# Kernel tuning notes

Measured on AMD Instinct MI355X. Metric: run time of the kernel, lower is better.

The kernel has to match this reference:

```python
import jax, jax.numpy as jnp
import numpy as np
import math

NUM_HEADS = 8
DIM = 512
HEAD_DIM = DIM // NUM_HEADS
SCALE = HEAD_DIM ** -0.5
RP = 2            # remove_pad = kernel_size//2 * 2 for kernel_size=3
EPS_GN = 1e-5     # GroupNorm eps
EPS_L1 = 1e-12    # F.normalize eps


def _conv(x, w, b):
    # x: [B, Cin, H, W], w: [Cout, Cin, 3, 3] (OIHW), VALID padding, stride 1
    y = jax.lax.conv_general_dilated(x, w, (1, 1), 'VALID',
                                     dimension_numbers=('NCHW', 'OIHW', 'NCHW'))
    return y + b[None, :, None, None]


def _gn_per_channel(x, g, b):
    # GroupNorm with num_groups == num_channels: per-channel norm over (H, W)
    mu = x.mean(axis=(-2, -1), keepdims=True)
    var = x.var(axis=(-2, -1), keepdims=True)
    xn = (x - mu) * jax.lax.rsqrt(var + EPS_GN)
    return xn * g[None, :, None, None] + b[None, :, None, None]


def _ppe(rpe, c1w, c1b, g1w, g1b, c2w, c2b, g2w, g2b):
    # PeripheralPositionEncoding: rpe [side^2, side^2, 4*H] -> [1, H, N, N], N=(side-2*RP)^2
    nr, _, d = rpe.shape
    side = int(round(math.sqrt(nr)))
    s2 = side - 2 * RP
    x = rpe.reshape(side, side, side, side, d)          # i j k l d
    x = x[RP:side - RP, RP:side - RP]                   # trim i, j borders
    x = x.transpose(0, 1, 4, 2, 3).reshape(s2 * s2, d, side, side)  # (ij) d k l
    x = jax.nn.relu(_gn_per_channel(_conv(x, c1w, c1b), g1w, g1b))
    x = _gn_per_channel(_conv(x, c2w, c2b), g2w, g2b)   # [(ij), H, s2, s2]
    y = x.reshape(s2 * s2, NUM_HEADS, s2 * s2).transpose(1, 0, 2)[None]  # [1,H,N,N]
    return jax.nn.sigmoid(y)


def setup_inputs() -> dict:
    key = jax.random.key(0)
    ks = jax.random.split(key, 12)
    B, N = 8, 1024            # N = (36 - 4)^2
    side = 36
    cin = NUM_HEADS * 4       # 32
    inp = {
        'x': jax.random.normal(ks[0], (B, N, DIM), jnp.float32),
        'rpe_embed': jax.random.normal(ks[1], (side * side, side * side, cin), jnp.float32),
        'wqkv': jax.random.normal(ks[2], (3 * DIM, DIM), jnp.float32) * 0.02,
        'wproj': jax.random.normal(ks[3], (DIM, DIM), jnp.float32) * 0.02,
        'bproj': jnp.zeros((DIM,), jnp.float32),
        'c1w': jax.random.normal(ks[4], (cin, cin, 3, 3), jnp.float32) * 0.02,
        'c1b': jnp.zeros((cin,), jnp.float32),
        'g1w': jnp.ones((cin,), jnp.float32),
        'g1b': jnp.zeros((cin,), jnp.float32),
        'c2w': jax.random.normal(ks[5], (NUM_HEADS, cin, 3, 3), jnp.float32) * 0.02,
        'c2b': jnp.zeros((NUM_HEADS,), jnp.float32),
        'g2w': jnp.ones((NUM_HEADS,), jnp.float32),        # norm_init[1] = 1.0
        'g2b': jnp.zeros((NUM_HEADS,), jnp.float32),       # norm_init[0] = 0.0
    }
    return inp


def reference(x, rpe_embed, wqkv, wproj, bproj, c1w, c1b, g1w, g1b, c2w, c2b, g2w, g2b):
    B, N, D = x.shape
    H, HD = NUM_HEADS, HEAD_DIM
    qkv = x @ wqkv.T                                   # [B, N, 3D]
    q, k, v = jnp.split(qkv, 3, axis=-1)
    def heads(t):
        return t.reshape(B, N, H, HD).transpose(0, 2, 1, 3)  # [B, H, N, HD]
    q, k, v = heads(q), heads(k), heads(v)
    dots = jnp.einsum('bhnd,bhmd->bhnm', q, k) * SCALE
    dots = jnp.exp(dots - dots.max(axis=-1, keepdims=True))  # stable exp-score
    w = _ppe(rpe_embed, c1w, c1b, g1w, g1b, c2w, c2b, g2w, g2b)  # [1,H,N,N]
    attn = w * dots
    attn = attn / jnp.maximum(jnp.abs(attn).sum(axis=-1, keepdims=True), EPS_L1)  # L1 normalize
    out = jnp.einsum('bhnm,bhmd->bhnd', attn, v)
    out = out.transpose(0, 2, 1, 3).reshape(B, N, D)
    return out @ wproj.T + bproj
```

## Files before the change

### kernel.cpp

```cpp
#include <hip/hip_runtime.h>
#include <hip/hip_fp16.h>


typedef __attribute__((ext_vector_type(8))) short bf16x8;
typedef __attribute__((ext_vector_type(8))) _Float16 f16x8;
typedef __attribute__((ext_vector_type(4))) float f32x4;

__device__ __forceinline__ unsigned short f2bf(float f) {
  unsigned u = __builtin_bit_cast(unsigned, f);
  u += 0x7FFFu + ((u >> 16) & 1u);
  return (unsigned short)(u >> 16);
}

__global__ __launch_bounds__(256) void wprep(
    const float* __restrict__ c1w, const float* __restrict__ c2w,
    unsigned short* __restrict__ w1frag, unsigned short* __restrict__ w2frag)
{
  int t = blockIdx.x * 256 + threadIdx.x;
  if (t < 9216) {
    int j = t & 7, ln = (t >> 3) & 63, ctap = t >> 9;
    int tap = ctap >> 1, ct = ctap & 1;
    int oc = 2 * (ln & 15) + ct, ic = (ln >> 4) * 8 + j;
    w1frag[t] = __half_as_ushort(__float2half(c1w[(oc * 32 + ic) * 9 + tap]));
  }
  if (t < 4608) {
    int j = t & 7, ln = (t >> 3) & 63, tap = t >> 9;
    int oc = (ln & 15) & 7, ic = (ln >> 4) * 8 + j;
    w2frag[t] = __half_as_ushort(__float2half(c2w[(oc * 32 + ic) * 9 + tap]));
  }
}

__global__ __launch_bounds__(256) void wcvt(
    const float* __restrict__ wqkv, const float* __restrict__ wproj,
    __half* __restrict__ wqkvh, __half* __restrict__ wprojh)
{
  int t = blockIdx.x * 256 + threadIdx.x;
  if (t < 196608) {
    float4 v = ((const float4*)wqkv)[t];
    __half2 h0 = __floats2half2_rn(v.x, v.y);
    __half2 h1 = __floats2half2_rn(v.z, v.w);
    uint2 u; u.x = __builtin_bit_cast(unsigned, h0); u.y = __builtin_bit_cast(unsigned, h1);
    *(uint2*)&wqkvh[t * 4] = u;
  } else {
    int t2 = t - 196608;
    float4 v = ((const float4*)wproj)[t2];
    __half2 h0 = __floats2half2_rn(v.x, v.y);
    __half2 h1 = __floats2half2_rn(v.z, v.w);
    uint2 u; u.x = __builtin_bit_cast(unsigned, h0); u.y = __builtin_bit_cast(unsigned, h1);
    *(uint2*)&wprojh[t2 * 4] = u;
  }
}

template<bool A_HALF, bool OUT_BF16>
__global__ __launch_bounds__(256) void gemm_f16_bt(
    const void* __restrict__ Av, const __half* __restrict__ Bh,
    void* __restrict__ Cv, const float* __restrict__ bias,
    int M, int N, int K)
{
  __shared__ __align__(16) _Float16 As[128 * 40];
  __shared__ __align__(16) _Float16 Bs[128 * 40];
  const int tid = threadIdx.x;
  const int wv = tid >> 6, ln = tid & 63, lr = ln & 15, lq = ln >> 4;
  const int wm = wv >> 1, wn = wv & 1;
  const int m0 = blockIdx.y * 128, n0 = blockIdx.x * 128;

  f32x4 acc[4][4];
#pragma unroll
  for (int i = 0; i < 4; i++)
#pragma unroll
    for (int j = 0; j < 4; j++) acc[i][j] = (f32x4){0.f, 0.f, 0.f, 0.f};

  const int sr = tid >> 1, sk = (tid & 1) * 16;
  const float*  Af = (const float*)Av;
  const __half* Ah = (const __half*)Av;

  for (int k0 = 0; k0 < K; k0 += 32) {
    uint4 ha0, ha1;
    float4 av0, av1, av2, av3;
    if (A_HALF) {
      ha0 = *(const uint4*)(Ah + (size_t)(m0 + sr) * K + k0 + sk);
      ha1 = *(const uint4*)(Ah + (size_t)(m0 + sr) * K + k0 + sk + 8);
    } else {
      const float* Ap = Af + (size_t)(m0 + sr) * K + k0 + sk;
      av0 = *(const float4*)(Ap);      av1 = *(const float4*)(Ap + 4);
      av2 = *(const float4*)(Ap + 8);  av3 = *(const float4*)(Ap + 12);
    }
    uint4 hb0 = *(const uint4*)(Bh + (size_t)(n0 + sr) * K + k0 + sk);
    uint4 hb1 = *(const uint4*)(Bh + (size_t)(n0 + sr) * K + k0 + sk + 8);
    __syncthreads();
    if (A_HALF) {
      *(uint4*)&As[sr * 40 + sk] = ha0;
      *(uint4*)&As[sr * 40 + sk + 8] = ha1;
    } else {
      f16x8 p0, p1;
      p0[0]=(_Float16)av0.x; p0[1]=(_Float16)av0.y; p0[2]=(_Float16)av0.z; p0[3]=(_Float16)av0.w;
      p0[4]=(_Float16)av1.x; p0[5]=(_Float16)av1.y; p0[6]=(_Float16)av1.z; p0[7]=(_Float16)av1.w;
      p1[0]=(_Float16)av2.x; p1[1]=(_Float16)av2.y; p1[2]=(_Float16)av2.z; p1[3]=(_Float16)av2.w;
      p1[4]=(_Float16)av3.x; p1[5]=(_Float16)av3.y; p1[6]=(_Float16)av3.z; p1[7]=(_Float16)av3.w;
      *(f16x8*)&As[sr * 40 + sk] = p0;
      *(f16x8*)&As[sr * 40 + sk + 8] = p1;
    }
    *(uint4*)&Bs[sr * 40 + sk] = hb0;
    *(uint4*)&Bs[sr * 40 + sk + 8] = hb1;
    __syncthreads();
    f16x8 af[4], bf[4];
#pragma unroll
    for (int mf = 0; mf < 4; mf++)
      af[mf] = *(const f16x8*)&As[(wm * 64 + mf * 16 + lr) * 40 + lq * 8];
#pragma unroll
    for (int nf = 0; nf < 4; nf++)
      bf[nf] = *(const f16x8*)&Bs[(wn * 64 + nf * 16 + lr) * 40 + lq * 8];
#pragma unroll
    for (int mf = 0; mf < 4; mf++)
#pragma unroll
      for (int nf = 0; nf < 4; nf++)
        acc[mf][nf] = __builtin_amdgcn_mfma_f32_16x16x32_f16(af[mf], bf[nf], acc[mf][nf], 0, 0, 0);
  }

#pragma unroll
  for (int mf = 0; mf < 4; mf++)
#pragma unroll
    for (int reg = 0; reg < 4; reg++) {
      const int row = m0 + wm * 64 + mf * 16 + lq * 4 + reg;
#pragma unroll
      for (int nf = 0; nf < 4; nf++) {
        const int col = n0 + wn * 64 + nf * 16 + lr;
        float v = acc[mf][nf][reg];
        if (bias) v += bias[col];
        if (OUT_BF16) ((unsigned short*)Cv)[(size_t)row * N + col] = f2bf(v);
        else          ((float*)Cv)[(size_t)row * N + col] = v;
      }
    }
}

__global__ __launch_bounds__(1024, 1) void conv_fused3(
    const float* __restrict__ rpe,
    const unsigned short* __restrict__ w1frag, const unsigned short* __restrict__ w2frag,
    const float* __restrict__ g1, const float* __restrict__ b1,
    const float* __restrict__ g2, const float* __restrict__ b2,
    __half* __restrict__ wout)
{
  extern __shared__ __align__(16) char smem[];
  unsigned short* inA = (unsigned short*)smem;
  unsigned short* yB  = (unsigned short*)(smem + 82944);
  float* statA = (float*)(smem + 156928);
  float* aL    = (float*)(smem + 157184);
  float* cL    = aL + 32;
  float* transF = (float*)smem;

  const int tid = threadIdx.x;
  const int wv = tid >> 6, ln = tid & 63;
  const int lr = ln & 15, lq = ln >> 4;
  const int p = blockIdx.x;

  if (tid < 64) statA[tid] = 0.f;

  const float* src = rpe + (size_t)(((p >> 5) + 2) * 36 + (p & 31) + 2) * 41472;
  for (int t = tid; t < 10368; t += 1024) {
    int pix = t >> 3, dq = (t & 7) << 2;
    float4 v = *(const float4*)(src + pix * 32 + dq);
    __half2 h0 = __floats2half2_rn(v.x, v.y);
    __half2 h1 = __floats2half2_rn(v.z, v.w);
    uint2 u; u.x = __builtin_bit_cast(unsigned, h0); u.y = __builtin_bit_cast(unsigned, h1);
    *(uint2*)&inA[(dq >> 3) * 10368 + pix * 8 + (dq & 7)] = u;
  }

  f16x8 w1f[2][9];
#pragma unroll
  for (int ct = 0; ct < 2; ct++)
#pragma unroll
    for (int tap = 0; tap < 9; tap++)
      w1f[ct][tap] = *(const f16x8*)&w1frag[((tap * 2 + ct) * 64 + ln) * 8];
  __syncthreads();

  constexpr int OFF1[9] = {0, 8, 16, 288, 296, 304, 576, 584, 592};
  const unsigned short* inAg = inA + lq * 10368;
  float s0 = 0.f, q0 = 0.f, s1 = 0.f, q1 = 0.f;
  for (int t0 = wv; t0 < 64; t0 += 32) {
    const int tA = t0, tB = t0 + 16;
    const int mA = tA * 16 + lr, mB = tB * 16 + lr;
    const unsigned short* abA = inAg + ((mA / 34) * 36 + (mA % 34)) * 8;
    const unsigned short* abB = inAg + ((mB / 34) * 36 + (mB % 34)) * 8;
    f32x4 cA0 = {0.f,0.f,0.f,0.f}, cA1 = {0.f,0.f,0.f,0.f};
    f32x4 cB0 = {0.f,0.f,0.f,0.f}, cB1 = {0.f,0.f,0.f,0.f};
#pragma unroll
    for (int tap = 0; tap < 9; tap++) {
      f16x8 avA = *(const f16x8*)(abA + OFF1[tap]);
      f16x8 avB = *(const f16x8*)(abB + OFF1[tap]);
      cA0 = __builtin_amdgcn_mfma_f32_16x16x32_f16(avA, w1f[0][tap], cA0, 0, 0, 0);
      cA1 = __builtin_amdgcn_mfma_f32_16x16x32_f16(avA, w1f[1][tap], cA1, 0, 0, 0);
      cB0 = __builtin_amdgcn_mfma_f32_16x16x32_f16(avB, w1f[0][tap], cB0, 0, 0, 0);
      cB1 = __builtin_amdgcn_mfma_f32_16x16x32_f16(avB, w1f[1][tap], cB1, 0, 0, 0);
    }
#pragma unroll
    for (int r = 0; r < 4; r++) {
      int moA = tA * 16 + lq * 4 + r;
      float v0 = cA0[r], v1 = cA1[r];
      unsigned u = (unsigned)__half_as_ushort(__float2half(v0))
                 | ((unsigned)__half_as_ushort(__float2half(v1)) << 16);
      *(unsigned*)&yB[(lr >> 2) * 9248 + moA * 8 + ((lr * 2) & 7)] = u;
      s0 += v0; q0 += v0 * v0; s1 += v1; q1 += v1 * v1;
      int moB = tB * 16 + lq * 4 + r;
      float w0 = cB0[r], w1 = cB1[r];
      unsigned u2 = (unsigned)__half_as_ushort(__float2half(w0))
                  | ((unsigned)__half_as_ushort(__float2half(w1)) << 16);
      *(unsigned*)&yB[(lr >> 2) * 9248 + moB * 8 + ((lr * 2) & 7)] = u2;
      s0 += w0; q0 += w0 * w0; s1 += w1; q1 += w1 * w1;
    }
  }
  if (wv < 9) {
    int t = wv + 64;
    int m = t * 16 + lr;
    int ms = m < 1155 ? m : 1155;
    const unsigned short* ab = inAg + ((ms / 34) * 36 + (ms % 34)) * 8;
    f32x4 c0 = {0.f,0.f,0.f,0.f}, c1v = {0.f,0.f,0.f,0.f};
#pragma unroll
    for (int tap = 0; tap < 9; tap++) {
      f16x8 av = *(const f16x8*)(ab + OFF1[tap]);
      c0  = __builtin_amdgcn_mfma_f32_16x16x32_f16(av, w1f[0][tap], c0, 0, 0, 0);
      c1v = __builtin_amdgcn_mfma_f32_16x16x32_f16(av, w1f[1][tap], c1v, 0, 0, 0);
    }
#pragma unroll
    for (int r = 0; r < 4; r++) {
      int mo = t * 16 + lq * 4 + r;
      if (mo < 1156) {
        float v0 = c0[r], v1 = c1v[r];
        unsigned u = (unsigned)__half_as_ushort(__float2half(v0))
                   | ((unsigned)__half_as_ushort(__float2half(v1)) << 16);
        *(unsigned*)&yB[(lr >> 2) * 9248 + mo * 8 + ((lr * 2) & 7)] = u;
        s0 += v0; q0 += v0 * v0; s1 += v1; q1 += v1 * v1;
      }
    }
  }
#pragma unroll
  for (int off = 16; off < 64; off <<= 1) {
    s0 += __shfl_xor(s0, off); q0 += __shfl_xor(q0, off);
    s1 += __shfl_xor(s1, off); q1 += __shfl_xor(q1, off);
  }
  if (ln < 16) {
    atomicAdd(&statA[ln], s0);      atomicAdd(&statA[16 + ln], q0);
    atomicAdd(&statA[32 + ln], s1); atomicAdd(&statA[48 + ln], q1);
  }
  __syncthreads();
  if (tid < 32) {
    int cti = tid >> 4, lri = tid & 15;
    float s = statA[cti * 32 + lri];
    float q = statA[cti * 32 + 16 + lri];
    int ch = 2 * lri + cti;
    float mu = s * (1.f / 1156.f);
    float var = q * (1.f / 1156.f) - mu * mu;
    float a_ = rsqrtf(var + 1e-5f) * g1[ch];
    aL[ch] = a_; cL[ch] = b1[ch] - mu * a_;
  }
  if (tid < 16) statA[tid] = 0.f;
  __syncthreads();

  {
    int g = tid >> 8, ocb = g * 8;
    unsigned short* yg = yB + g * 9248;
    for (int pix = (tid & 255); pix < 1156; pix += 256) {
      f16x8 raw = *(const f16x8*)&yg[pix * 8];
      f16x8 outv;
#pragma unroll
      for (int e = 0; e < 8; e++) {
        float v = (float)raw[e];
        outv[e] = (_Float16)fmaxf(v * aL[ocb + e] + cL[ocb + e], 0.f);
      }
      *(f16x8*)&yg[pix * 8] = outv;
    }
  }
  __syncthreads();

  f16x8 w2f[9];
#pragma unroll
  for (int tap = 0; tap < 9; tap++)
    w2f[tap] = *(const f16x8*)&w2frag[(tap * 64 + ln) * 8];

  constexpr int OFF2[9] = {0, 8, 16, 272, 280, 288, 544, 552, 560};
  const unsigned short* yBg = yB + lq * 9248;
  float s2 = 0.f, q2 = 0.f;
#pragma unroll
  for (int t0 = 0; t0 < 2; t0++) {
    const int tA = wv + t0 * 32, tB = tA + 16;
    const int mA = tA * 16 + lr, mB = tB * 16 + lr;
    const unsigned short* abA = yBg + ((mA >> 5) * 34 + (mA & 31)) * 8;
    const unsigned short* abB = yBg + ((mB >> 5) * 34 + (mB & 31)) * 8;
    f32x4 ccA = {0.f,0.f,0.f,0.f}, ccB = {0.f,0.f,0.f,0.f};
#pragma unroll
    for (int tap = 0; tap < 9; tap++) {
      f16x8 avA = *(const f16x8*)(abA + OFF2[tap]);
      f16x8 avB = *(const f16x8*)(abB + OFF2[tap]);
      ccA = __builtin_amdgcn_mfma_f32_16x16x32_f16(avA, w2f[tap], ccA, 0, 0, 0);
      ccB = __builtin_amdgcn_mfma_f32_16x16x32_f16(avB, w2f[tap], ccB, 0, 0, 0);
    }
#pragma unroll
    for (int r = 0; r < 4; r++) {
      float vA = ccA[r], vB = ccB[r];
      s2 += vA + vB; q2 += vA * vA + vB * vB;
      if (lr < 8) {
        transF[lr * 1032 + tA * 16 + lq * 4 + r] = vA;
        transF[lr * 1032 + tB * 16 + lq * 4 + r] = vB;
      }
    }
  }
#pragma unroll
  for (int off = 16; off < 64; off <<= 1) {
    s2 += __shfl_xor(s2, off); q2 += __shfl_xor(q2, off);
  }
  if (ln < 8) { atomicAdd(&statA[ln], s2); atomicAdd(&statA[8 + ln], q2); }
  __syncthreads();
  if (tid < 8) {
    float s = statA[tid], q = statA[8 + tid];
    float mu = s * (1.f / 1024.f);
    float var = q * (1.f / 1024.f) - mu * mu;
    float a_ = rsqrtf(var + 1e-5f) * g2[tid];
    aL[tid] = a_; cL[tid] = b2[tid] - mu * a_;
  }
  __syncthreads();

  {
    int oc = tid >> 7, p8 = (tid & 127) << 3;
    float a_ = aL[oc], c_ = cL[oc];
    f16x8 o;
#pragma unroll
    for (int e = 0; e < 8; e++) {
      float v = transF[oc * 1032 + p8 + e];
      o[e] = (_Float16)(1.f / (1.f + __expf(-(v * a_ + c_))));
    }
    *(f16x8*)&wout[((size_t)oc << 20) + ((size_t)p << 10) + p8] = o;
  }
}

__global__ __launch_bounds__(256) void attn_kernel(
    const unsigned short* __restrict__ qkv,
    const __half* __restrict__ wppe,
    __half* __restrict__ oh)
{
  __shared__ __align__(16) unsigned short k_lds[64 * 72];
  __shared__ __align__(16) unsigned short v_lds[64 * 72];
  __shared__ __align__(16) unsigned short p_lds[4 * 16 * 72];
  const int tid = threadIdx.x;
  const int wv = tid >> 6, ln = tid & 63;
  const int lr = ln & 15, lq = ln >> 4;
  const int b = blockIdx.y >> 3, h = blockIdx.y & 7;
  const int n0 = blockIdx.x << 6;

  const size_t qoff = (size_t)((b << 10) + n0 + (wv << 4) + lr) * 1536 + (h << 6);
  bf16x8 qf0 = *(const bf16x8*)(qkv + qoff + lq * 8);
  bf16x8 qf1 = *(const bf16x8*)(qkv + qoff + 32 + lq * 8);

  f32x4 acc[4];
#pragma unroll
  for (int dt = 0; dt < 4; dt++) acc[dt] = (f32x4){0.f, 0.f, 0.f, 0.f};
  float den[4] = {0.f, 0.f, 0.f, 0.f};
  const __half* wp = wppe + ((size_t)h << 20);

  for (int m0 = 0; m0 < 1024; m0 += 64) {
    __syncthreads();
    for (int t = tid; t < 512; t += 256) {
      int m = t >> 3, dq = t & 7;
      const unsigned short* kr = qkv + (size_t)((b << 10) + m0 + m) * 1536 + 512 + (h << 6) + dq * 8;
      *(uint4*)&k_lds[m * 72 + dq * 8] = *(const uint4*)kr;
      uint4 vvv = *(const uint4*)(kr + 512);
      unsigned short tmp[8];
      *(uint4*)tmp = vvv;
#pragma unroll
      for (int i = 0; i < 8; i++) {
        int d = dq * 8 + i;
        v_lds[d * 72 + (m ^ (((d >> 3) & 7) << 3))] = tmp[i];
      }
    }
    __syncthreads();

    f32x4 s[4];
#pragma unroll
    for (int mt = 0; mt < 4; mt++) {
      const unsigned short* kb = &k_lds[(mt * 16 + lr) * 72 + lq * 8];
      f32x4 cz = (f32x4){0.f, 0.f, 0.f, 0.f};
      cz = __builtin_amdgcn_mfma_f32_16x16x32_bf16(qf0, *(const bf16x8*)kb, cz, 0, 0, 0);
      cz = __builtin_amdgcn_mfma_f32_16x16x32_bf16(qf1, *(const bf16x8*)(kb + 32), cz, 0, 0, 0);
      s[mt] = cz;
    }
#pragma unroll
    for (int mt = 0; mt < 4; mt++)
#pragma unroll
      for (int reg = 0; reg < 4; reg++) {
        int rrow = lq * 4 + reg;
        float wvl = __half2float(wp[(size_t)(n0 + (wv << 4) + rrow) * 1024 + (m0 + mt * 16 + lr)]);
        float pv = wvl * __expf(s[mt][reg] * 0.125f);
        den[reg] += pv;
        p_lds[((wv << 4) + rrow) * 72 + mt * 16 + lr] = f2bf(pv);
      }
    const unsigned short* pb = &p_lds[((wv << 4) + lr) * 72];
    bf16x8 pa0 = *(const bf16x8*)(pb + lq * 8);
    bf16x8 pa1 = *(const bf16x8*)(pb + 32 + lq * 8);
#pragma unroll
    for (int dt = 0; dt < 4; dt++) {
      int d = dt * 16 + lr;
      int sw = ((d >> 3) & 7) << 3;
      const unsigned short* vb = &v_lds[d * 72];
      acc[dt] = __builtin_amdgcn_mfma_f32_16x16x32_bf16(pa0, *(const bf16x8*)(vb + ((lq * 8) ^ sw)), acc[dt], 0, 0, 0);
      acc[dt] = __builtin_amdgcn_mfma_f32_16x16x32_bf16(pa1, *(const bf16x8*)(vb + ((32 + lq * 8) ^ sw)), acc[dt], 0, 0, 0);
    }
  }
#pragma unroll
  for (int off = 1; off < 16; off <<= 1)
#pragma unroll
    for (int reg = 0; reg < 4; reg++) den[reg] += __shfl_xor(den[reg], off);
#pragma unroll
  for (int dt = 0; dt < 4; dt++)
#pragma unroll
    for (int reg = 0; reg < 4; reg++) {
      size_t row = (size_t)((b << 10) + n0 + (wv << 4) + lq * 4 + reg);
      oh[row * 512 + (h << 6) + dt * 16 + lr] = __float2half(acc[dt][reg] / den[reg]);
    }
}

extern "C" void kernel_launch(void* const* d_in, const int* in_sizes, int n_in,
                              void* d_out, int out_size, void* d_ws, size_t ws_size,
                              hipStream_t stream) {
  (void)in_sizes; (void)n_in; (void)out_size; (void)ws_size;
  const float* x     = (const float*)d_in[0];
  const float* rpe   = (const float*)d_in[1];
  const float* wqkv  = (const float*)d_in[2];
  const float* wproj = (const float*)d_in[3];
  const float* bproj = (const float*)d_in[4];
  const float* c1w   = (const float*)d_in[5];
  const float* g1w   = (const float*)d_in[7];
  const float* g1b   = (const float*)d_in[8];
  const float* c2w   = (const float*)d_in[9];
  const float* g2w   = (const float*)d_in[11];
  const float* g2b   = (const float*)d_in[12];
  float* out = (float*)d_out;

  char* ws = (char*)d_ws;
  unsigned short* qkv_bf = (unsigned short*)ws;
  __half* wppe_h = (__half*)(ws + 25165824);
  __half* oh_h   = (__half*)(ws + 41943040);
  unsigned short* w1frag = (unsigned short*)(ws + 50331648);
  unsigned short* w2frag = (unsigned short*)(ws + 50350080);
  __half* wqkvh  = (__half*)(ws + 50359296);
  __half* wprojh = (__half*)(ws + 51932160);

  wprep<<<36, 256, 0, stream>>>(c1w, c2w, w1frag, w2frag);
  wcvt<<<1024, 256, 0, stream>>>(wqkv, wproj, wqkvh, wprojh);

  gemm_f16_bt<false, true><<<dim3(12, 64), 256, 0, stream>>>(
      x, wqkvh, qkv_bf, nullptr, 8192, 1536, 512);

  const int ldsC = 157440;
  hipFuncSetAttribute(reinterpret_cast<const void*>(&conv_fused3),
                      hipFuncAttributeMaxDynamicSharedMemorySize, ldsC);
  conv_fused3<<<1024, 1024, ldsC, stream>>>(rpe, w1frag, w2frag, g1w, g1b, g2w, g2b, wppe_h);

  attn_kernel<<<dim3(16, 64), 256, 0, stream>>>(qkv_bf, wppe_h, oh_h);

  gemm_f16_bt<true, false><<<dim3(4, 64), 256, 0, stream>>>(
      oh_h, wprojh, out, bproj, 8192, 512, 512);
}
```

Before: 193.6 us.

## Read conv1 inputs directly from global memory, dropping the LDS staging buffer

The first convolution now loads its fp32 rpe inputs straight from global memory per tap and converts them to fp16 in registers, instead of staging the whole input tile in LDS first. This removes the 83KB input buffer, shrinking LDS so the compiler hint allows more than one block per CU. The conv2 results are kept in registers and written to the reused transpose buffer only after the stats barrier, which avoids overwriting the aliased LDS region too early. The cost is redundant global reads, each input pixel fetched up to nine times and relying on cache, plus higher register pressure from holding the raw tap values.

```diff
diff --git a/kernel.cpp b/kernel.cpp
--- a/kernel.cpp
+++ b/kernel.cpp
@@ -133,7 +133,7 @@
     }
 }
 
-__global__ __launch_bounds__(1024, 1) void conv_fused3(
+__global__ __launch_bounds__(1024, 8) void conv_fused4(
     const float* __restrict__ rpe,
     const unsigned short* __restrict__ w1frag, const unsigned short* __restrict__ w2frag,
     const float* __restrict__ g1, const float* __restrict__ b1,
@@ -141,11 +141,10 @@
     __half* __restrict__ wout)
 {
   extern __shared__ __align__(16) char smem[];
-  unsigned short* inA = (unsigned short*)smem;
-  unsigned short* yB  = (unsigned short*)(smem + 82944);
-  float* statA = (float*)(smem + 156928);
-  float* aL    = (float*)(smem + 157184);
-  float* cL    = aL + 32;
+  unsigned short* yB  = (unsigned short*)smem;
+  float* statA = (float*)(smem + 73984);
+  float* aL    = (float*)(smem + 74240);
+  float* cL    = (float*)(smem + 74368);
   float* transF = (float*)smem;
 
   const int tid = threadIdx.x;
@@ -155,16 +154,6 @@
 
   if (tid < 64) statA[tid] = 0.f;
 
-  const float* src = rpe + (size_t)(((p >> 5) + 2) * 36 + (p & 31) + 2) * 41472;
-  for (int t = tid; t < 10368; t += 1024) {
-    int pix = t >> 3, dq = (t & 7) << 2;
-    float4 v = *(const float4*)(src + pix * 32 + dq);
-    __half2 h0 = __floats2half2_rn(v.x, v.y);
-    __half2 h1 = __floats2half2_rn(v.z, v.w);
-    uint2 u; u.x = __builtin_bit_cast(unsigned, h0); u.y = __builtin_bit_cast(unsigned, h1);
-    *(uint2*)&inA[(dq >> 3) * 10368 + pix * 8 + (dq & 7)] = u;
-  }
-
   f16x8 w1f[2][9];
 #pragma unroll
   for (int ct = 0; ct < 2; ct++)
@@ -173,50 +162,27 @@
       w1f[ct][tap] = *(const f16x8*)&w1frag[((tap * 2 + ct) * 64 + ln) * 8];
   __syncthreads();
 
-  constexpr int OFF1[9] = {0, 8, 16, 288, 296, 304, 576, 584, 592};
-  const unsigned short* inAg = inA + lq * 10368;
+  const float* src = rpe + (size_t)(((p >> 5) + 2) * 36 + (p & 31) + 2) * 41472;
+  constexpr int OFF1G[9] = {0, 32, 64, 1152, 1184, 1216, 2304, 2336, 2368};
   float s0 = 0.f, q0 = 0.f, s1 = 0.f, q1 = 0.f;
-  for (int t0 = wv; t0 < 64; t0 += 32) {
-    const int tA = t0, tB = t0 + 16;
-    const int mA = tA * 16 + lr, mB = tB * 16 + lr;
-    const unsigned short* abA = inAg + ((mA / 34) * 36 + (mA % 34)) * 8;
-    const unsigned short* abB = inAg + ((mB / 34) * 36 + (mB % 34)) * 8;
-    f32x4 cA0 = {0.f,0.f,0.f,0.f}, cA1 = {0.f,0.f,0.f,0.f};
-    f32x4 cB0 = {0.f,0.f,0.f,0.f}, cB1 = {0.f,0.f,0.f,0.f};
-#pragma unroll
-    for (int tap = 0; tap < 9; tap++) {
-      f16x8 avA = *(const f16x8*)(abA + OFF1[tap]);
-      f16x8 avB = *(const f16x8*)(abB + OFF1[tap]);
-      cA0 = __builtin_amdgcn_mfma_f32_16x16x32_f16(avA, w1f[0][tap], cA0, 0, 0, 0);
-      cA1 = __builtin_amdgcn_mfma_f32_16x16x32_f16(avA, w1f[1][tap], cA1, 0, 0, 0);
-      cB0 = __builtin_amdgcn_mfma_f32_16x16x32_f16(avB, w1f[0][tap], cB0, 0, 0, 0);
-      cB1 = __builtin_amdgcn_mfma_f32_16x16x32_f16(avB, w1f[1][tap], cB1, 0, 0, 0);
-    }
-#pragma unroll
-    for (int r = 0; r < 4; r++) {
-      int moA = tA * 16 + lq * 4 + r;
-      float v0 = cA0[r], v1 = cA1[r];
-      unsigned u = (unsigned)__half_as_ushort(__float2half(v0))
-                 | ((unsigned)__half_as_ushort(__float2half(v1)) << 16);
-      *(unsigned*)&yB[(lr >> 2) * 9248 + moA * 8 + ((lr * 2) & 7)] = u;
-      s0 += v0; q0 += v0 * v0; s1 += v1; q1 += v1 * v1;
-      int moB = tB * 16 + lq * 4 + r;
-      float w0 = cB0[r], w1 = cB1[r];
-      unsigned u2 = (unsigned)__half_as_ushort(__float2half(w0))
-                  | ((unsigned)__half_as_ushort(__float2half(w1)) << 16);
-      *(unsigned*)&yB[(lr >> 2) * 9248 + moB * 8 + ((lr * 2) & 7)] = u2;
-      s0 += w0; q0 += w0 * w0; s1 += w1; q1 += w1 * w1;
-    }
-  }
-  if (wv < 9) {
-    int t = wv + 64;
+  for (int t = wv; t < 73; t += 16) {
     int m = t * 16 + lr;
     int ms = m < 1155 ? m : 1155;
-    const unsigned short* ab = inAg + ((ms / 34) * 36 + (ms % 34)) * 8;
+    const float* ab = src + ((ms / 34) * 36 + (ms % 34)) * 32 + lq * 8;
+    float4 raw0[9], raw1[9];
+#pragma unroll
+    for (int tap = 0; tap < 9; tap++) {
+      raw0[tap] = *(const float4*)(ab + OFF1G[tap]);
+      raw1[tap] = *(const float4*)(ab + OFF1G[tap] + 4);
+    }
     f32x4 c0 = {0.f,0.f,0.f,0.f}, c1v = {0.f,0.f,0.f,0.f};
 #pragma unroll
     for (int tap = 0; tap < 9; tap++) {
-      f16x8 av = *(const f16x8*)(ab + OFF1[tap]);
+      f16x8 av;
+      av[0]=(_Float16)raw0[tap].x; av[1]=(_Float16)raw0[tap].y;
+      av[2]=(_Float16)raw0[tap].z; av[3]=(_Float16)raw0[tap].w;
+      av[4]=(_Float16)raw1[tap].x; av[5]=(_Float16)raw1[tap].y;
+      av[6]=(_Float16)raw1[tap].z; av[7]=(_Float16)raw1[tap].w;
       c0  = __builtin_amdgcn_mfma_f32_16x16x32_f16(av, w1f[0][tap], c0, 0, 0, 0);
       c1v = __builtin_amdgcn_mfma_f32_16x16x32_f16(av, w1f[1][tap], c1v, 0, 0, 0);
     }
@@ -272,12 +238,14 @@
   __syncthreads();
 
   f16x8 w2f[9];
+  const int ic0 = lq * 8;
 #pragma unroll
   for (int tap = 0; tap < 9; tap++)
     w2f[tap] = *(const f16x8*)&w2frag[(tap * 64 + ln) * 8];
 
   constexpr int OFF2[9] = {0, 8, 16, 272, 280, 288, 544, 552, 560};
   const unsigned short* yBg = yB + lq * 9248;
+  f32x4 zsave[4];
   float s2 = 0.f, q2 = 0.f;
 #pragma unroll
   for (int t0 = 0; t0 < 2; t0++) {
@@ -293,14 +261,11 @@
       ccA = __builtin_amdgcn_mfma_f32_16x16x32_f16(avA, w2f[tap], ccA, 0, 0, 0);
       ccB = __builtin_amdgcn_mfma_f32_16x16x32_f16(avB, w2f[tap], ccB, 0, 0, 0);
     }
+    zsave[t0 * 2] = ccA; zsave[t0 * 2 + 1] = ccB;
 #pragma unroll
     for (int r = 0; r < 4; r++) {
       float vA = ccA[r], vB = ccB[r];
       s2 += vA + vB; q2 += vA * vA + vB * vB;
-      if (lr < 8) {
-        transF[lr * 1032 + tA * 16 + lq * 4 + r] = vA;
-        transF[lr * 1032 + tB * 16 + lq * 4 + r] = vB;
-      }
     }
   }
 #pragma unroll
@@ -309,6 +274,18 @@
   }
   if (ln < 8) { atomicAdd(&statA[ln], s2); atomicAdd(&statA[8 + ln], q2); }
   __syncthreads();
+
+  if (lr < 8) {
+#pragma unroll
+    for (int t0 = 0; t0 < 2; t0++) {
+      const int tA = wv + t0 * 32, tB = tA + 16;
+#pragma unroll
+      for (int r = 0; r < 4; r++) {
+        transF[lr * 1032 + tA * 16 + lq * 4 + r] = zsave[t0 * 2][r];
+        transF[lr * 1032 + tB * 16 + lq * 4 + r] = zsave[t0 * 2 + 1][r];
+      }
+    }
+  }
   if (tid < 8) {
     float s = statA[tid], q = statA[8 + tid];
     float mu = s * (1.f / 1024.f);
@@ -448,10 +425,10 @@
   gemm_f16_bt<false, true><<<dim3(12, 64), 256, 0, stream>>>(
       x, wqkvh, qkv_bf, nullptr, 8192, 1536, 512);
 
-  const int ldsC = 157440;
-  hipFuncSetAttribute(reinterpret_cast<const void*>(&conv_fused3),
+  const int ldsC = 74496;
+  hipFuncSetAttribute(reinterpret_cast<const void*>(&conv_fused4),
                       hipFuncAttributeMaxDynamicSharedMemorySize, ldsC);
-  conv_fused3<<<1024, 1024, ldsC, stream>>>(rpe, w1frag, w2frag, g1w, g1b, g2w, g2b, wppe_h);
+  conv_fused4<<<1024, 1024, ldsC, stream>>>(rpe, w1frag, w2frag, g1w, g1b, g2w, g2b, wppe_h);
 
   attn_kernel<<<dim3(16, 64), 256, 0, stream>>>(qkv_bf, wppe_h, oh_h);
 
```

Measured after the change: 417.8 us. 116% more time.
